# Performance work log

Measured on AMD Instinct MI355X. Metric: run time of the kernel, lower is better.

Reference implementation:

```python
import jax, jax.numpy as jnp
import numpy as np

C = 128          # num_channels
S = 3000         # sequence_num
INTER = 30
EXTRACT = S // INTER  # 100
EPS = 1e-5


def _layernorm(y, g, b):
    # LayerNorm over last (channel) axis, eps=1e-5 like torch default
    m = jnp.mean(y, axis=-1, keepdims=True)
    v = jnp.mean(jnp.square(y - m), axis=-1, keepdims=True)
    return (y - m) * jax.lax.rsqrt(v + EPS) * g + b


def setup_inputs() -> dict:
    key = jax.random.key(0)
    ks = jax.random.split(key, 4)
    x = jax.random.normal(ks[0], (32, 4, C, S), dtype=jnp.float32)
    # xavier_normal Linear weights, zero bias; LayerNorm gamma=1, beta=0
    std = float(np.sqrt(2.0 / (C + C)))
    def lin_w(k):
        return jax.random.normal(k, (C, C), dtype=jnp.float32) * std
    Wq = lin_w(ks[1]); Wk = lin_w(ks[2]); Wp = lin_w(ks[3])
    z = jnp.zeros((C,), jnp.float32); o = jnp.ones((C,), jnp.float32)
    return {
        "x": x,
        "Wq": Wq, "bq": z, "gq": o, "betaq": z,
        "Wk": Wk, "bk": z, "gk": o, "betak": z,
        "Wp": Wp, "bp": z, "gp": o, "betap": z,
    }


def reference(x, Wq, bq, gq, betaq, Wk, bk, gk, betak, Wp, bp, gp, betap):
    # x: [b, o, c, s]
    temp = jnp.swapaxes(x, -1, -2)                         # [b,o,s,c]
    q = _layernorm(temp @ Wq.T + bq, gq, betaq)            # [b,o,s,c]
    k = _layernorm(temp @ Wk.T + bk, gk, betak)            # [b,o,s,c]
    q = jnp.swapaxes(q, -1, -2)                            # [b,o,c,s]
    k = jnp.swapaxes(k, -1, -2)                            # [b,o,c,s]
    scaling = jnp.asarray(EXTRACT, x.dtype) ** 0.5         # sqrt(extract_sequence)
    atten = jnp.einsum('bocs,boms->bocm', q, k) / scaling  # [b,o,c,c]
    score = jax.nn.softmax(atten, axis=-1)                 # [b,o,c,c]
    # faithful to source: contracts m (score rows sum to 1)
    out = jnp.einsum('bocs,bocm->bocs', x, score)          # [b,o,c,s]
    out = jnp.swapaxes(out, -1, -2)                        # [b,o,s,c]
    out = _layernorm(out @ Wp.T + bp, gp, betap)
    return jnp.swapaxes(out, -1, -2)                       # [b,o,c,s]
```

## Files before the change

### kernel.cpp

```cpp
#include <hip/hip_runtime.h>
#include <hip/hip_bf16.h>


#define C    128
#define SEQ  3000
#define NG   128
#define NT   128
#define NBLK ((SEQ + NT - 1) / NT)

typedef float f4 __attribute__((ext_vector_type(4)));
typedef short short8 __attribute__((ext_vector_type(8)));

__device__ __forceinline__ unsigned short f2bf(float f) {
    union { float f; unsigned u; } v; v.f = f;
    unsigned r = v.u + 0x7fffu + ((v.u >> 16) & 1u);
    return (unsigned short)(r >> 16);
}

__device__ __forceinline__ int swz(int row, int chunk) {
    return chunk ^ ((row ^ (row >> 2)) & 15);
}

__global__ void cvt_wp(const float* __restrict__ Wp, unsigned short* __restrict__ out) {
    int i = blockIdx.x * 256 + threadIdx.x;
    if (i < C * C) out[i] = f2bf(Wp[i]);
}

__global__ __launch_bounds__(256, 2) void gemm_ln_mfma(
    const float* __restrict__ x,
    const unsigned short* __restrict__ wbf,
    const float* __restrict__ bp,
    const float* __restrict__ gp,
    const float* __restrict__ bep,
    float* __restrict__ out)
{
    __shared__ __align__(16) unsigned short Wl[C * C];
    __shared__ __align__(16) unsigned short Xl[NT * C];

    const int g  = blockIdx.y;
    const int s0 = blockIdx.x * NT;
    const float* xg = x + (size_t)g * (C * SEQ);
    float* og = out + (size_t)g * (C * SEQ);
    const int t = threadIdx.x;

    {
        const uint4* wsrc = (const uint4*)wbf;
        #pragma unroll
        for (int i = 0; i < 8; ++i) {
            int cid = t + 256 * i;
            int c  = cid >> 4;
            int ch = cid & 15;
            uint4 v = wsrc[cid];
            *(uint4*)&Wl[c * C + swz(c, ch) * 8] = v;
        }
    }

    {
        const int sq  = t & 31;
        const int mcb = t >> 5;
        const int s_loc  = 4 * sq;
        const int s_glob = s0 + s_loc;
        const bool valid = (s_glob + 3) < SEQ;
        #pragma unroll
        for (int half = 0; half < 2; ++half) {
            const int mc = mcb + 8 * half;
            f4 r[8];
            const float* xp = xg + (size_t)(mc * 8) * SEQ + s_glob;
            #pragma unroll
            for (int rr = 0; rr < 8; ++rr) {
                if (valid) r[rr] = *(const f4*)(xp + (size_t)rr * SEQ);
                else       r[rr] = (f4){0.f, 0.f, 0.f, 0.f};
            }
            #pragma unroll
            for (int j = 0; j < 4; ++j) {
                const int sl = s_loc + j;
                uint4 pk;
                pk.x = (unsigned)f2bf(r[0][j]) | ((unsigned)f2bf(r[1][j]) << 16);
                pk.y = (unsigned)f2bf(r[2][j]) | ((unsigned)f2bf(r[3][j]) << 16);
                pk.z = (unsigned)f2bf(r[4][j]) | ((unsigned)f2bf(r[5][j]) << 16);
                pk.w = (unsigned)f2bf(r[6][j]) | ((unsigned)f2bf(r[7][j]) << 16);
                *(uint4*)&Xl[sl * C + swz(sl, mc) * 8] = pk;
            }
        }
    }
    __syncthreads();

    const int w    = t >> 6;
    const int lane = t & 63;
    const int col  = lane & 15;
    const int quad = lane >> 4;

    f4 acc[2][8];
    #pragma unroll
    for (int nt = 0; nt < 2; ++nt)
        #pragma unroll
        for (int mt = 0; mt < 8; ++mt) acc[nt][mt] = (f4){0.f, 0.f, 0.f, 0.f};

    #pragma unroll
    for (int kc = 0; kc < 4; ++kc) {
        short8 a[8], b[2];
        #pragma unroll
        for (int mt = 0; mt < 8; ++mt) {
            const int row = 16 * mt + col;
            a[mt] = *(const short8*)&Wl[row * C + swz(row, 4 * kc + quad) * 8];
        }
        #pragma unroll
        for (int nt = 0; nt < 2; ++nt) {
            const int srow = 32 * w + 16 * nt + col;
            b[nt] = *(const short8*)&Xl[srow * C + swz(srow, 4 * kc + quad) * 8];
        }
        #pragma unroll
        for (int nt = 0; nt < 2; ++nt)
            #pragma unroll
            for (int mt = 0; mt < 8; ++mt)
                acc[nt][mt] = __builtin_amdgcn_mfma_f32_16x16x32_bf16(
                    a[mt], b[nt], acc[nt][mt], 0, 0, 0);
    }

    #pragma unroll
    for (int mt = 0; mt < 8; ++mt) {
        const f4 b4 = *(const f4*)(bp + 16 * mt + 4 * quad);
        #pragma unroll
        for (int nt = 0; nt < 2; ++nt)
            #pragma unroll
            for (int r = 0; r < 4; ++r) acc[nt][mt][r] += b4[r];
    }

    float mean[2], rstd[2];
    #pragma unroll
    for (int nt = 0; nt < 2; ++nt) {
        float s = 0.f, q = 0.f;
        #pragma unroll
        for (int mt = 0; mt < 8; ++mt)
            #pragma unroll
            for (int r = 0; r < 4; ++r) {
                float y = acc[nt][mt][r];
                s += y; q += y * y;
            }
        s += __shfl_xor(s, 16); q += __shfl_xor(q, 16);
        s += __shfl_xor(s, 32); q += __shfl_xor(q, 32);
        float m = s * (1.0f / C);
        float v = q * (1.0f / C) - m * m;
        mean[nt] = m;
        rstd[nt] = rsqrtf(v + 1e-5f);
    }

    #pragma unroll
    for (int mt = 0; mt < 8; ++mt) {
        const f4 g4 = *(const f4*)(gp  + 16 * mt + 4 * quad);
        const f4 e4 = *(const f4*)(bep + 16 * mt + 4 * quad);
        #pragma unroll
        for (int nt = 0; nt < 2; ++nt) {
            const int sg = s0 + 32 * w + 16 * nt + col;
            if (sg < SEQ) {
                #pragma unroll
                for (int r = 0; r < 4; ++r) {
                    const int c = 16 * mt + 4 * quad + r;
                    og[(size_t)c * SEQ + sg] =
                        (acc[nt][mt][r] - mean[nt]) * rstd[nt] * g4[r] + e4[r];
                }
            }
        }
    }
}

extern "C" void kernel_launch(void* const* d_in, const int* in_sizes, int n_in,
                              void* d_out, int out_size, void* d_ws, size_t ws_size,
                              hipStream_t stream) {
    const float* x   = (const float*)d_in[0];
    const float* Wp  = (const float*)d_in[9];
    const float* bp  = (const float*)d_in[10];
    const float* gp  = (const float*)d_in[11];
    const float* bep = (const float*)d_in[12];
    float* out = (float*)d_out;
    unsigned short* wbf = (unsigned short*)d_ws;

    hipLaunchKernelGGL(cvt_wp, dim3(64), dim3(256), 0, stream, Wp, wbf);

    dim3 grid(NBLK, NG);
    hipLaunchKernelGGL(gemm_ln_mfma, grid, dim3(256), 0, stream,
                       x, wbf, bp, gp, bep, out);
}
```

Measured before the change: 399.3 us.

## Read weights from global memory, swap MFMA operands for vectorized stores, use packed bf16 convert

Drops the shared-memory copy of the bf16 weight matrix; each lane now loads its weight fragments straight from global memory (L2/L1 cached), which halves LDS use and allows four blocks per CU. The MFMA operands are swapped so each lane's accumulators hold four consecutive sequence positions for one channel. That makes the LayerNorm reduction a 16-lane shuffle and lets outputs be written as float4 stores instead of scalar stores. The fp32-to-bf16 packing uses the hardware v_cvt_pk_bf16_f32 instruction. The trade-off is repeated global weight loads per block and less unrolling of the K loop.

```diff
diff --git a/kernel.cpp b/kernel.cpp
--- a/kernel.cpp
+++ b/kernel.cpp
@@ -1,5 +1,4 @@
 #include <hip/hip_runtime.h>
-#include <hip/hip_bf16.h>
 
 
 #define C    128
@@ -17,6 +16,12 @@
     return (unsigned short)(r >> 16);
 }
 
+__device__ __forceinline__ unsigned cvt2(float lo, float hi) {
+    unsigned r;
+    asm("v_cvt_pk_bf16_f32 %0, %1, %2" : "=v"(r) : "v"(lo), "v"(hi));
+    return r;
+}
+
 __device__ __forceinline__ int swz(int row, int chunk) {
     return chunk ^ ((row ^ (row >> 2)) & 15);
 }
@@ -26,7 +31,7 @@
     if (i < C * C) out[i] = f2bf(Wp[i]);
 }
 
-__global__ __launch_bounds__(256, 2) void gemm_ln_mfma(
+__global__ __launch_bounds__(256, 4) void gemm_ln_mfma(
     const float* __restrict__ x,
     const unsigned short* __restrict__ wbf,
     const float* __restrict__ bp,
@@ -34,7 +39,6 @@
     const float* __restrict__ bep,
     float* __restrict__ out)
 {
-    __shared__ __align__(16) unsigned short Wl[C * C];
     __shared__ __align__(16) unsigned short Xl[NT * C];
 
     const int g  = blockIdx.y;
@@ -42,18 +46,6 @@
     const float* xg = x + (size_t)g * (C * SEQ);
     float* og = out + (size_t)g * (C * SEQ);
     const int t = threadIdx.x;
-
-    {
-        const uint4* wsrc = (const uint4*)wbf;
-        #pragma unroll
-        for (int i = 0; i < 8; ++i) {
-            int cid = t + 256 * i;
-            int c  = cid >> 4;
-            int ch = cid & 15;
-            uint4 v = wsrc[cid];
-            *(uint4*)&Wl[c * C + swz(c, ch) * 8] = v;
-        }
-    }
 
     {
         const int sq  = t & 31;
@@ -75,10 +67,10 @@
             for (int j = 0; j < 4; ++j) {
                 const int sl = s_loc + j;
                 uint4 pk;
-                pk.x = (unsigned)f2bf(r[0][j]) | ((unsigned)f2bf(r[1][j]) << 16);
-                pk.y = (unsigned)f2bf(r[2][j]) | ((unsigned)f2bf(r[3][j]) << 16);
-                pk.z = (unsigned)f2bf(r[4][j]) | ((unsigned)f2bf(r[5][j]) << 16);
-                pk.w = (unsigned)f2bf(r[6][j]) | ((unsigned)f2bf(r[7][j]) << 16);
+                pk.x = cvt2(r[0][j], r[1][j]);
+                pk.y = cvt2(r[2][j], r[3][j]);
+                pk.z = cvt2(r[4][j], r[5][j]);
+                pk.w = cvt2(r[6][j], r[7][j]);
                 *(uint4*)&Xl[sl * C + swz(sl, mc) * 8] = pk;
             }
         }
@@ -96,69 +88,74 @@
         #pragma unroll
         for (int mt = 0; mt < 8; ++mt) acc[nt][mt] = (f4){0.f, 0.f, 0.f, 0.f};
 
-    #pragma unroll
+    const unsigned short* wl = wbf + col * C + quad * 8;
+
+    #pragma unroll 1
     for (int kc = 0; kc < 4; ++kc) {
-        short8 a[8], b[2];
-        #pragma unroll
-        for (int mt = 0; mt < 8; ++mt) {
-            const int row = 16 * mt + col;
-            a[mt] = *(const short8*)&Wl[row * C + swz(row, 4 * kc + quad) * 8];
-        }
+        short8 a[2], b[8];
         #pragma unroll
         for (int nt = 0; nt < 2; ++nt) {
             const int srow = 32 * w + 16 * nt + col;
-            b[nt] = *(const short8*)&Xl[srow * C + swz(srow, 4 * kc + quad) * 8];
+            a[nt] = *(const short8*)&Xl[srow * C + swz(srow, 4 * kc + quad) * 8];
         }
+        #pragma unroll
+        for (int mt = 0; mt < 8; ++mt)
+            b[mt] = *(const short8*)(wl + mt * 16 * C + kc * 32);
         #pragma unroll
         for (int nt = 0; nt < 2; ++nt)
             #pragma unroll
             for (int mt = 0; mt < 8; ++mt)
                 acc[nt][mt] = __builtin_amdgcn_mfma_f32_16x16x32_bf16(
-                    a[mt], b[nt], acc[nt][mt], 0, 0, 0);
+                    a[nt], b[mt], acc[nt][mt], 0, 0, 0);
+    }
+
+    float bl[8], gl[8], el[8];
+    #pragma unroll
+    for (int mt = 0; mt < 8; ++mt) {
+        const int c = 16 * mt + col;
+        bl[mt] = bp[c]; gl[mt] = gp[c]; el[mt] = bep[c];
     }
 
     #pragma unroll
-    for (int mt = 0; mt < 8; ++mt) {
-        const f4 b4 = *(const f4*)(bp + 16 * mt + 4 * quad);
-        #pragma unroll
-        for (int nt = 0; nt < 2; ++nt)
-            #pragma unroll
-            for (int r = 0; r < 4; ++r) acc[nt][mt][r] += b4[r];
-    }
-
-    float mean[2], rstd[2];
-    #pragma unroll
-    for (int nt = 0; nt < 2; ++nt) {
-        float s = 0.f, q = 0.f;
+    for (int nt = 0; nt < 2; ++nt)
         #pragma unroll
         for (int mt = 0; mt < 8; ++mt)
             #pragma unroll
-            for (int r = 0; r < 4; ++r) {
+            for (int r = 0; r < 4; ++r) acc[nt][mt][r] += bl[mt];
+
+    float mean[2][4], rstd[2][4];
+    #pragma unroll
+    for (int nt = 0; nt < 2; ++nt)
+        #pragma unroll
+        for (int r = 0; r < 4; ++r) {
+            float s = 0.f, q = 0.f;
+            #pragma unroll
+            for (int mt = 0; mt < 8; ++mt) {
                 float y = acc[nt][mt][r];
                 s += y; q += y * y;
             }
-        s += __shfl_xor(s, 16); q += __shfl_xor(q, 16);
-        s += __shfl_xor(s, 32); q += __shfl_xor(q, 32);
-        float m = s * (1.0f / C);
-        float v = q * (1.0f / C) - m * m;
-        mean[nt] = m;
-        rstd[nt] = rsqrtf(v + 1e-5f);
-    }
+            s += __shfl_xor(s, 1); q += __shfl_xor(q, 1);
+            s += __shfl_xor(s, 2); q += __shfl_xor(q, 2);
+            s += __shfl_xor(s, 4); q += __shfl_xor(q, 4);
+            s += __shfl_xor(s, 8); q += __shfl_xor(q, 8);
+            float m = s * (1.0f / C);
+            float v = q * (1.0f / C) - m * m;
+            mean[nt][r] = m;
+            rstd[nt][r] = rsqrtf(v + 1e-5f);
+        }
 
     #pragma unroll
-    for (int mt = 0; mt < 8; ++mt) {
-        const f4 g4 = *(const f4*)(gp  + 16 * mt + 4 * quad);
-        const f4 e4 = *(const f4*)(bep + 16 * mt + 4 * quad);
-        #pragma unroll
-        for (int nt = 0; nt < 2; ++nt) {
-            const int sg = s0 + 32 * w + 16 * nt + col;
-            if (sg < SEQ) {
+    for (int nt = 0; nt < 2; ++nt) {
+        const int sg = s0 + 32 * w + 16 * nt + 4 * quad;
+        if (sg < SEQ) {
+            #pragma unroll
+            for (int mt = 0; mt < 8; ++mt) {
+                const int c = 16 * mt + col;
+                f4 v;
                 #pragma unroll
-                for (int r = 0; r < 4; ++r) {
-                    const int c = 16 * mt + 4 * quad + r;
-                    og[(size_t)c * SEQ + sg] =
-                        (acc[nt][mt][r] - mean[nt]) * rstd[nt] * g4[r] + e4[r];
-                }
+                for (int r = 0; r < 4; ++r)
+                    v[r] = (acc[nt][mt][r] - mean[nt][r]) * rstd[nt][r] * gl[mt] + el[mt];
+                *(f4*)&og[(size_t)c * SEQ + sg] = v;
             }
         }
     }
```

Result: slower. 423.3 us (+6.0%).

## Make GEMM+LayerNorm persistent per wave with register prefetch of next tile

Applied to the files above, without the earlier changes.

The kernel now launches a fixed grid of 512 blocks whose waves each loop over 32-wide sequence tiles of one group. The next tile's x data is prefetched into registers while the current tile's MFMA and LayerNorm run, which is meant to hide global-load latency and cut per-block weight staging. Groups are mapped to blocks so that each XCD handles a contiguous set of groups. Weights are pre-swizzled once in the conversion kernel so the LDS fill becomes a plain copy, and activation conversion uses the packed bf16 convert instruction. The cost is more live registers for the prefetch buffers, and tail tiles rely on clamped loads plus masked stores.

```diff
diff --git a/kernel.cpp b/kernel.cpp
--- a/kernel.cpp
+++ b/kernel.cpp
@@ -1,12 +1,13 @@
 #include <hip/hip_runtime.h>
-#include <hip/hip_bf16.h>
 
 
 #define C    128
 #define SEQ  3000
 #define NG   128
-#define NT   128
-#define NBLK ((SEQ + NT - 1) / NT)
+#define ST   32
+#define SPG  ((SEQ + ST - 1) / ST)
+#define WPG  16
+#define GPX  16
 
 typedef float f4 __attribute__((ext_vector_type(4)));
 typedef short short8 __attribute__((ext_vector_type(8)));
@@ -17,13 +18,21 @@
     return (unsigned short)(r >> 16);
 }
 
+__device__ __forceinline__ unsigned cvt2(float lo, float hi) {
+    unsigned r;
+    asm("v_cvt_pk_bf16_f32 %0, %1, %2" : "=v"(r) : "v"(lo), "v"(hi));
+    return r;
+}
+
 __device__ __forceinline__ int swz(int row, int chunk) {
     return chunk ^ ((row ^ (row >> 2)) & 15);
 }
 
 __global__ void cvt_wp(const float* __restrict__ Wp, unsigned short* __restrict__ out) {
     int i = blockIdx.x * 256 + threadIdx.x;
-    if (i < C * C) out[i] = f2bf(Wp[i]);
+    if (i >= C * C) return;
+    int c = i >> 7, r = i & 127, ch = r >> 3, j = r & 7;
+    out[c * C + swz(c, ch) * 8 + j] = f2bf(Wp[i]);
 }
 
 __global__ __launch_bounds__(256, 2) void gemm_ln_mfma(
@@ -35,53 +44,15 @@
     float* __restrict__ out)
 {
     __shared__ __align__(16) unsigned short Wl[C * C];
-    __shared__ __align__(16) unsigned short Xl[NT * C];
-
-    const int g  = blockIdx.y;
-    const int s0 = blockIdx.x * NT;
-    const float* xg = x + (size_t)g * (C * SEQ);
-    float* og = out + (size_t)g * (C * SEQ);
+    __shared__ __align__(16) unsigned short Xs[4][ST * C];
+
     const int t = threadIdx.x;
 
     {
         const uint4* wsrc = (const uint4*)wbf;
-        #pragma unroll
-        for (int i = 0; i < 8; ++i) {
-            int cid = t + 256 * i;
-            int c  = cid >> 4;
-            int ch = cid & 15;
-            uint4 v = wsrc[cid];
-            *(uint4*)&Wl[c * C + swz(c, ch) * 8] = v;
-        }
-    }
-
-    {
-        const int sq  = t & 31;
-        const int mcb = t >> 5;
-        const int s_loc  = 4 * sq;
-        const int s_glob = s0 + s_loc;
-        const bool valid = (s_glob + 3) < SEQ;
-        #pragma unroll
-        for (int half = 0; half < 2; ++half) {
-            const int mc = mcb + 8 * half;
-            f4 r[8];
-            const float* xp = xg + (size_t)(mc * 8) * SEQ + s_glob;
-            #pragma unroll
-            for (int rr = 0; rr < 8; ++rr) {
-                if (valid) r[rr] = *(const f4*)(xp + (size_t)rr * SEQ);
-                else       r[rr] = (f4){0.f, 0.f, 0.f, 0.f};
-            }
-            #pragma unroll
-            for (int j = 0; j < 4; ++j) {
-                const int sl = s_loc + j;
-                uint4 pk;
-                pk.x = (unsigned)f2bf(r[0][j]) | ((unsigned)f2bf(r[1][j]) << 16);
-                pk.y = (unsigned)f2bf(r[2][j]) | ((unsigned)f2bf(r[3][j]) << 16);
-                pk.z = (unsigned)f2bf(r[4][j]) | ((unsigned)f2bf(r[5][j]) << 16);
-                pk.w = (unsigned)f2bf(r[6][j]) | ((unsigned)f2bf(r[7][j]) << 16);
-                *(uint4*)&Xl[sl * C + swz(sl, mc) * 8] = pk;
-            }
-        }
+        uint4* wdst = (uint4*)Wl;
+        #pragma unroll
+        for (int i = 0; i < 8; ++i) wdst[t + 256 * i] = wsrc[t + 256 * i];
     }
     __syncthreads();
 
@@ -89,75 +60,137 @@
     const int lane = t & 63;
     const int col  = lane & 15;
     const int quad = lane >> 4;
-
-    f4 acc[2][8];
-    #pragma unroll
-    for (int nt = 0; nt < 2; ++nt)
-        #pragma unroll
-        for (int mt = 0; mt < 8; ++mt) acc[nt][mt] = (f4){0.f, 0.f, 0.f, 0.f};
-
-    #pragma unroll
-    for (int kc = 0; kc < 4; ++kc) {
-        short8 a[8], b[2];
+    const int sq   = lane & 7;
+    const int mc   = lane >> 3;
+    unsigned short* X = &Xs[w][0];
+
+    const int b     = blockIdx.x;
+    const int xcd   = b & 7;
+    const int wx    = (b >> 3) * 4 + w;
+    const int g     = xcd * GPX + (wx >> 4);
+    const int gwave = wx & 15;
+    const float* xg = x   + (size_t)g * (C * SEQ);
+    float*       og = out + (size_t)g * (C * SEQ);
+
+    f4 r0[8], r1[8];
+    int sid = gwave;
+    {
+        int sb = sid * ST + 4 * sq;
+        const float* p0 = xg + (size_t)(mc * 8) * SEQ + sb;
+        const float* p1 = p0 + (size_t)64 * SEQ;
+        #pragma unroll
+        for (int rr = 0; rr < 8; ++rr) r0[rr] = *(const f4*)(p0 + (size_t)rr * SEQ);
+        #pragma unroll
+        for (int rr = 0; rr < 8; ++rr) r1[rr] = *(const f4*)(p1 + (size_t)rr * SEQ);
+    }
+
+    #pragma unroll 1
+    for (; sid < SPG; sid += WPG) {
+        const int s0 = sid * ST;
+
+        #pragma unroll
+        for (int j = 0; j < 4; ++j) {
+            const int sl = 4 * sq + j;
+            uint4 pk;
+            pk.x = cvt2(r0[0][j], r0[1][j]);
+            pk.y = cvt2(r0[2][j], r0[3][j]);
+            pk.z = cvt2(r0[4][j], r0[5][j]);
+            pk.w = cvt2(r0[6][j], r0[7][j]);
+            *(uint4*)&X[sl * C + swz(sl, mc) * 8] = pk;
+        }
+        #pragma unroll
+        for (int j = 0; j < 4; ++j) {
+            const int sl = 4 * sq + j;
+            uint4 pk;
+            pk.x = cvt2(r1[0][j], r1[1][j]);
+            pk.y = cvt2(r1[2][j], r1[3][j]);
+            pk.z = cvt2(r1[4][j], r1[5][j]);
+            pk.w = cvt2(r1[6][j], r1[7][j]);
+            *(uint4*)&X[sl * C + swz(sl, 8 + mc) * 8] = pk;
+        }
+
+        {
+            int nsid = sid + WPG; if (nsid >= SPG) nsid = sid;
+            int sb = nsid * ST + 4 * sq;
+            if (sb > SEQ - 4) sb = SEQ - 4;
+            const float* p0 = xg + (size_t)(mc * 8) * SEQ + sb;
+            const float* p1 = p0 + (size_t)64 * SEQ;
+            #pragma unroll
+            for (int rr = 0; rr < 8; ++rr) r0[rr] = *(const f4*)(p0 + (size_t)rr * SEQ);
+            #pragma unroll
+            for (int rr = 0; rr < 8; ++rr) r1[rr] = *(const f4*)(p1 + (size_t)rr * SEQ);
+        }
+
+        f4 acc[2][8];
+        #pragma unroll
+        for (int nt = 0; nt < 2; ++nt)
+            #pragma unroll
+            for (int mt = 0; mt < 8; ++mt) acc[nt][mt] = (f4){0.f, 0.f, 0.f, 0.f};
+
+        #pragma unroll 1
+        for (int kc = 0; kc < 4; ++kc) {
+            short8 xb[2];
+            #pragma unroll
+            for (int nt = 0; nt < 2; ++nt) {
+                const int row = nt * 16 + col;
+                xb[nt] = *(const short8*)&X[row * C + swz(row, 4 * kc + quad) * 8];
+            }
+            short8 a[8];
+            #pragma unroll
+            for (int mt = 0; mt < 8; ++mt) {
+                const int row = 16 * mt + col;
+                a[mt] = *(const short8*)&Wl[row * C + swz(row, 4 * kc + quad) * 8];
+            }
+            #pragma unroll
+            for (int nt = 0; nt < 2; ++nt)
+                #pragma unroll
+                for (int mt = 0; mt < 8; ++mt)
+                    acc[nt][mt] = __builtin_amdgcn_mfma_f32_16x16x32_bf16(
+                        a[mt], xb[nt], acc[nt][mt], 0, 0, 0);
+        }
+
         #pragma unroll
         for (int mt = 0; mt < 8; ++mt) {
-            const int row = 16 * mt + col;
-            a[mt] = *(const short8*)&Wl[row * C + swz(row, 4 * kc + quad) * 8];
-        }
+            const f4 b4 = *(const f4*)(bp + 16 * mt + 4 * quad);
+            #pragma unroll
+            for (int nt = 0; nt < 2; ++nt)
+                #pragma unroll
+                for (int rr = 0; rr < 4; ++rr) acc[nt][mt][rr] += b4[rr];
+        }
+
+        float mean[2], rstd[2];
         #pragma unroll
         for (int nt = 0; nt < 2; ++nt) {
-            const int srow = 32 * w + 16 * nt + col;
-            b[nt] = *(const short8*)&Xl[srow * C + swz(srow, 4 * kc + quad) * 8];
-        }
-        #pragma unroll
-        for (int nt = 0; nt < 2; ++nt)
+            float s = 0.f, q = 0.f;
             #pragma unroll
             for (int mt = 0; mt < 8; ++mt)
-                acc[nt][mt] = __builtin_amdgcn_mfma_f32_16x16x32_bf16(
-                    a[mt], b[nt], acc[nt][mt], 0, 0, 0);
-    }
-
-    #pragma unroll
-    for (int mt = 0; mt < 8; ++mt) {
-        const f4 b4 = *(const f4*)(bp + 16 * mt + 4 * quad);
-        #pragma unroll
-        for (int nt = 0; nt < 2; ++nt)
-            #pragma unroll
-            for (int r = 0; r < 4; ++r) acc[nt][mt][r] += b4[r];
-    }
-
-    float mean[2], rstd[2];
-    #pragma unroll
-    for (int nt = 0; nt < 2; ++nt) {
-        float s = 0.f, q = 0.f;
-        #pragma unroll
-        for (int mt = 0; mt < 8; ++mt)
-            #pragma unroll
-            for (int r = 0; r < 4; ++r) {
-                float y = acc[nt][mt][r];
-                s += y; q += y * y;
-            }
-        s += __shfl_xor(s, 16); q += __shfl_xor(q, 16);
-        s += __shfl_xor(s, 32); q += __shfl_xor(q, 32);
-        float m = s * (1.0f / C);
-        float v = q * (1.0f / C) - m * m;
-        mean[nt] = m;
-        rstd[nt] = rsqrtf(v + 1e-5f);
-    }
-
-    #pragma unroll
-    for (int mt = 0; mt < 8; ++mt) {
-        const f4 g4 = *(const f4*)(gp  + 16 * mt + 4 * quad);
-        const f4 e4 = *(const f4*)(bep + 16 * mt + 4 * quad);
-        #pragma unroll
-        for (int nt = 0; nt < 2; ++nt) {
-            const int sg = s0 + 32 * w + 16 * nt + col;
-            if (sg < SEQ) {
                 #pragma unroll
-                for (int r = 0; r < 4; ++r) {
-                    const int c = 16 * mt + 4 * quad + r;
-                    og[(size_t)c * SEQ + sg] =
-                        (acc[nt][mt][r] - mean[nt]) * rstd[nt] * g4[r] + e4[r];
+                for (int rr = 0; rr < 4; ++rr) {
+                    float y = acc[nt][mt][rr];
+                    s += y; q += y * y;
+                }
+            s += __shfl_xor(s, 16); q += __shfl_xor(q, 16);
+            s += __shfl_xor(s, 32); q += __shfl_xor(q, 32);
+            float m = s * (1.0f / C);
+            float v = q * (1.0f / C) - m * m;
+            mean[nt] = m;
+            rstd[nt] = rsqrtf(v + 1e-5f);
+        }
+
+        #pragma unroll
+        for (int mt = 0; mt < 8; ++mt) {
+            const f4 g4 = *(const f4*)(gp  + 16 * mt + 4 * quad);
+            const f4 e4 = *(const f4*)(bep + 16 * mt + 4 * quad);
+            #pragma unroll
+            for (int nt = 0; nt < 2; ++nt) {
+                const int sg = s0 + nt * 16 + col;
+                if (sg < SEQ) {
+                    #pragma unroll
+                    for (int rr = 0; rr < 4; ++rr) {
+                        const int c = 16 * mt + 4 * quad + rr;
+                        og[(size_t)c * SEQ + sg] =
+                            (acc[nt][mt][rr] - mean[nt]) * rstd[nt] * g4[rr] + e4[rr];
+                    }
                 }
             }
         }
@@ -177,7 +210,6 @@
 
     hipLaunchKernelGGL(cvt_wp, dim3(64), dim3(256), 0, stream, Wp, wbf);
 
-    dim3 grid(NBLK, NG);
-    hipLaunchKernelGGL(gemm_ln_mfma, grid, dim3(256), 0, stream,
+    hipLaunchKernelGGL(gemm_ln_mfma, dim3(512), dim3(256), 0, stream,
                        x, wbf, bp, gp, bep, out);
 }
```

After: 459.7 us. 15.1% more time.
